# Optimization experiments

Measured on AMD Instinct MI355X. Metric: run time of the kernel, lower is better.

Reference implementation:

```python
import jax, jax.numpy as jnp
import numpy as np
import math

NUM_HEADS = 32
NUM_KV_HEADS = 8
HEAD_DIM = 128
HIDDEN = 4096
BATCH = 2
SEQ = 2048
MASK_MIN = -1e9


def _rope(x, cos, sin):
    # x: [B, S, H, D], cos/sin: [S, D/2]
    d2 = x.shape[-1] // 2
    x1, x2 = x[..., :d2], x[..., d2:]
    c = cos[None, :, None, :]
    s = sin[None, :, None, :]
    return jnp.concatenate([x1 * c - x2 * s, x2 * c + x1 * s], axis=-1)


def setup_inputs() -> dict:
    key = jax.random.key(0)
    k1, k2, k3 = jax.random.split(key, 3)
    hidden_states = jax.random.normal(k1, (BATCH, SEQ, HIDDEN), dtype=jnp.float32) * 0.02
    Wqkv = jax.random.normal(k2, (HIDDEN, (NUM_HEADS + 2 * NUM_KV_HEADS) * HEAD_DIM), dtype=jnp.float32) * (HIDDEN ** -0.5)
    Wo = jax.random.normal(k3, (NUM_HEADS * HEAD_DIM, HIDDEN), dtype=jnp.float32) * (HIDDEN ** -0.5)
    pos = np.arange(SEQ, dtype=np.float32)
    inv_freq = 1.0 / (10000.0 ** (np.arange(0, HEAD_DIM, 2, dtype=np.float32) / HEAD_DIM))
    freqs = np.outer(pos, inv_freq)  # [S, D/2]
    cos = jnp.asarray(np.cos(freqs), dtype=jnp.float32)
    sin = jnp.asarray(np.sin(freqs), dtype=jnp.float32)
    # causal additive mask [B, 1, S, S]
    causal = np.triu(np.full((SEQ, SEQ), MASK_MIN, dtype=np.float32), k=1)
    attention_mask = jnp.broadcast_to(jnp.asarray(causal)[None, None], (BATCH, 1, SEQ, SEQ))
    return {"hidden_states": hidden_states, "Wqkv": Wqkv, "Wo": Wo,
            "cos": cos, "sin": sin, "attention_mask": attention_mask}


def reference(hidden_states, Wqkv, Wo, cos, sin, attention_mask):
    B, S, H = hidden_states.shape
    n_rep = NUM_HEADS // NUM_KV_HEADS
    qkv = jnp.einsum('bsh,hd->bsd', hidden_states, Wqkv)
    q_end = NUM_HEADS * HEAD_DIM
    k_end = q_end + NUM_KV_HEADS * HEAD_DIM
    q = qkv[..., :q_end].reshape(B, S, NUM_HEADS, HEAD_DIM)
    k = qkv[..., q_end:k_end].reshape(B, S, NUM_KV_HEADS, HEAD_DIM)
    v = qkv[..., k_end:].reshape(B, S, NUM_KV_HEADS, HEAD_DIM)
    q = _rope(q, cos, sin)
    k = _rope(k, cos, sin)
    # repeat_kv: expand kv heads to query heads
    k = jnp.repeat(k, n_rep, axis=2)  # [B, S, NH, D]
    v = jnp.repeat(v, n_rep, axis=2)
    scores = jnp.einsum('bqhd,bkhd->bhqk', q, k) / math.sqrt(HEAD_DIM)
    scores = scores + attention_mask
    scores = jnp.maximum(scores, jnp.finfo(scores.dtype).min)
    probs = jax.nn.softmax(scores.astype(jnp.float32), axis=-1).astype(q.dtype)
    attn = jnp.einsum('bhqk,bkhd->bqhd', probs, v)  # [B, S, NH, D]
    attn = attn.reshape(B, S, NUM_HEADS * HEAD_DIM)
    return jnp.einsum('bsd,dh->bsh', attn, Wo)
```

## Files before the change

### kernel.cpp

```cpp
#include <hip/hip_runtime.h>

typedef unsigned short u16;
typedef __bf16 bf16x8 __attribute__((ext_vector_type(8)));
typedef float f32x4 __attribute__((ext_vector_type(4)));
typedef float f32x16 __attribute__((ext_vector_type(16)));
typedef u16 u16x4 __attribute__((ext_vector_type(4)));

#define SEQ 2048
#define NQKV 6144
#define HID 4096

__device__ inline u16 f2bf(float f) {
  union { float f; unsigned u; } x; x.f = f;
  unsigned r = x.u + 0x7fffu + ((x.u >> 16) & 1u);
  return (u16)(r >> 16);
}
__device__ inline float bf2f(u16 u) {
  union { unsigned u; float f; } x; x.u = ((unsigned)u) << 16;
  return x.f;
}
__device__ inline f32x4 mfma16(bf16x8 a, bf16x8 b, f32x4 c) {
  return __builtin_amdgcn_mfma_f32_16x16x32_bf16(a, b, c, 0, 0, 0);
}
__device__ inline f32x16 mfma32(bf16x8 a, bf16x8 b, f32x16 c) {
  return __builtin_amdgcn_mfma_f32_32x32x16_bf16(a, b, c, 0, 0, 0);
}
__device__ inline unsigned cvtpk(float lo, float hi) {
  unsigned r;
  asm("v_cvt_pk_bf16_f32 %0, %1, %2" : "=v"(r) : "v"(lo), "v"(hi));
  return r;
}
__device__ inline void gload16(const void* g, void* l) {
  __builtin_amdgcn_global_load_lds((const __attribute__((address_space(1))) void*)g,
                                   (__attribute__((address_space(3))) void*)l,
                                   16, 0, 0);
}


__global__ __launch_bounds__(256) void conv_kernel(const float* __restrict__ in,
                                                   u16* __restrict__ out) {
  int i = (blockIdx.x * 256 + threadIdx.x) * 4;
  int m = i >> 12, k = i & 4095;
  float4 v = *(const float4*)(in + i);
  u16x4 o;
  o[0] = f2bf(v.x); o[1] = f2bf(v.y); o[2] = f2bf(v.z); o[3] = f2bf(v.w);
  int p = m >> 8, r = m & 255;
  int t = k >> 5, kc = (k >> 3) & 3, e = k & 7;
  int slot = ((r >> 5) << 7) + (kc << 5) + (r & 31);
  *(u16x4*)(out + ((size_t)(p * 128 + t) * 1024 + slot) * 8 + e) = o;
}

__global__ __launch_bounds__(256) void transconv_qkv_kernel(const float* __restrict__ in,
                                                            u16* __restrict__ out) {
  __shared__ u16 tile[32][33];
  int c0 = blockIdx.x * 32, r0 = blockIdx.y * 32;
  int tx = threadIdx.x & 31, ty = threadIdx.x >> 5;
  for (int i = 0; i < 4; ++i)
    tile[ty + 8 * i][tx] = f2bf(in[(size_t)(r0 + ty + 8 * i) * NQKV + c0 + tx]);
  __syncthreads();
  int t = r0 >> 5;
  for (int i = 0; i < 4; ++i) {
    int n = c0 + ty + 8 * i;
    int p = n / 384, pc = n - p * 384;
    int kc = tx >> 3, e = tx & 7;
    int slot = ((pc >> 5) << 7) + (kc << 5) + (pc & 31);
    out[((size_t)(p * 128 + t) * 1536 + slot) * 8 + e] = tile[tx][ty + 8 * i];
  }
}

__global__ __launch_bounds__(256) void transconv_kernel(const float* __restrict__ in,
                                                        u16* __restrict__ out,
                                                        int R, int C) {
  __shared__ u16 tile[32][33];
  int c0 = blockIdx.x * 32, r0 = blockIdx.y * 32;
  int tx = threadIdx.x & 31, ty = threadIdx.x >> 5;
  for (int i = 0; i < 4; ++i)
    tile[ty + 8 * i][tx] = f2bf(in[(size_t)(r0 + ty + 8 * i) * C + c0 + tx]);
  __syncthreads();
  for (int i = 0; i < 4; ++i)
    out[(size_t)(c0 + ty + 8 * i) * R + r0 + tx] = tile[tx][ty + 8 * i];
}

__global__ __launch_bounds__(512, 2) void gemm32_kernel(const u16* __restrict__ At,
                                                        const u16* __restrict__ Btl,
                                                        u16* __restrict__ C,
                                                        int M, int N, int K, int nby) {
  __shared__ __align__(16) u16 As[3][256 * 32];
  __shared__ __align__(16) u16 Bs[3][384 * 32];
  int nwg = gridDim.x;
  int bid = blockIdx.x;
  int s = (bid & 7) * (nwg >> 3) + (bid >> 3);
  int by = s % nby, bx = s / nby;
  int row0 = by * 256, col0 = bx * 384;
  int tid = threadIdx.x, w = tid >> 6, l = tid & 63;
  int wm = w >> 2, wn = w & 3;
  int l31 = l & 31, lh = l >> 5;
  const u16* Ap = At + (size_t)by * 128 * 1024 * 8;
  const u16* Bp = Btl + (size_t)bx * 128 * 1536 * 8;
  int nkt = K >> 5;

  f32x16 acc[4][3] = {};

#define STA32(tt, bf)                                                         \
  { _Pragma("unroll")                                                         \
    for (int j = 0; j < 2; ++j) {                                             \
      int cid = j * 512 + tid;                                                \
      gload16(Ap + ((size_t)(tt) * 1024 + cid) * 8, &As[bf][cid * 8]);        \
    } }
#define STB32(tt, bf)                                                         \
  { _Pragma("unroll")                                                         \
    for (int j = 0; j < 3; ++j) {                                             \
      int cid = j * 512 + tid;                                                \
      gload16(Bp + ((size_t)(tt) * 1536 + cid) * 8, &Bs[bf][cid * 8]);        \
    } }
#define RA32(bf, im, ks, dst)                                                 \
  { int slot = ((wm * 4 + (im)) << 7) + (((ks) * 2 + lh) << 5) + l31;         \
    dst = *(const bf16x8*)&As[bf][slot * 8]; }
#define RB32(bf, in, ks, dst)                                                 \
  { int slot = ((wn * 3 + (in)) << 7) + (((ks) * 2 + lh) << 5) + l31;         \
    dst = *(const bf16x8*)&Bs[bf][slot * 8]; }

  STA32(0, 0); STB32(0, 0); STA32(1, 1); STB32(1, 1);
  asm volatile("s_waitcnt vmcnt(5)" ::: "memory");
  __builtin_amdgcn_s_barrier();

  int cur = 0;
  for (int t = 0; t < nkt; ++t) {
    int nb = cur + 2; if (nb >= 3) nb -= 3;
    bool pf = (t + 2 < nkt);
    bf16x8 a0, a1, a2, a3, b0, b1, b2;
    RA32(cur, 0, 0, a0); RA32(cur, 1, 0, a1); RA32(cur, 2, 0, a2); RA32(cur, 3, 0, a3);
    RB32(cur, 0, 0, b0); RB32(cur, 1, 0, b1); RB32(cur, 2, 0, b2);
    if (pf) STA32(t + 2, nb);
    __builtin_amdgcn_s_barrier();
    asm volatile("s_waitcnt lgkmcnt(0)" ::: "memory");
    __builtin_amdgcn_s_setprio(1);
    acc[0][0] = mfma32(a0, b0, acc[0][0]); acc[0][1] = mfma32(a0, b1, acc[0][1]);
    acc[0][2] = mfma32(a0, b2, acc[0][2]);
    acc[1][0] = mfma32(a1, b0, acc[1][0]); acc[1][1] = mfma32(a1, b1, acc[1][1]);
    acc[1][2] = mfma32(a1, b2, acc[1][2]);
    acc[2][0] = mfma32(a2, b0, acc[2][0]); acc[2][1] = mfma32(a2, b1, acc[2][1]);
    acc[2][2] = mfma32(a2, b2, acc[2][2]);
    acc[3][0] = mfma32(a3, b0, acc[3][0]); acc[3][1] = mfma32(a3, b1, acc[3][1]);
    acc[3][2] = mfma32(a3, b2, acc[3][2]);
    __builtin_amdgcn_s_setprio(0);
    __builtin_amdgcn_s_barrier();
    RA32(cur, 0, 1, a0); RA32(cur, 1, 1, a1); RA32(cur, 2, 1, a2); RA32(cur, 3, 1, a3);
    RB32(cur, 0, 1, b0); RB32(cur, 1, 1, b1); RB32(cur, 2, 1, b2);
    if (pf) STB32(t + 2, nb);
    __builtin_amdgcn_s_barrier();
    asm volatile("s_waitcnt lgkmcnt(0)" ::: "memory");
    __builtin_amdgcn_s_setprio(1);
    acc[0][0] = mfma32(a0, b0, acc[0][0]); acc[0][1] = mfma32(a0, b1, acc[0][1]);
    acc[0][2] = mfma32(a0, b2, acc[0][2]);
    acc[1][0] = mfma32(a1, b0, acc[1][0]); acc[1][1] = mfma32(a1, b1, acc[1][1]);
    acc[1][2] = mfma32(a1, b2, acc[1][2]);
    acc[2][0] = mfma32(a2, b0, acc[2][0]); acc[2][1] = mfma32(a2, b1, acc[2][1]);
    acc[2][2] = mfma32(a2, b2, acc[2][2]);
    acc[3][0] = mfma32(a3, b0, acc[3][0]); acc[3][1] = mfma32(a3, b1, acc[3][1]);
    acc[3][2] = mfma32(a3, b2, acc[3][2]);
    __builtin_amdgcn_s_setprio(0);
    if (pf)              { asm volatile("s_waitcnt vmcnt(5)" ::: "memory"); }
    else if (t + 1 < nkt){ asm volatile("s_waitcnt vmcnt(0)" ::: "memory"); }
    __builtin_amdgcn_s_barrier();
    cur = cur + 1 == 3 ? 0 : cur + 1;
  }
#undef STA32
#undef STB32
#undef RA32
#undef RB32

#pragma unroll
  for (int im = 0; im < 4; ++im)
#pragma unroll
    for (int in = 0; in < 3; ++in)
#pragma unroll
      for (int reg = 0; reg < 16; ++reg) {
        int row = row0 + wm * 128 + im * 32 + (reg & 3) + 8 * (reg >> 2) + 4 * lh;
        int col = col0 + wn * 96 + in * 32 + l31;
        C[(size_t)row * N + col] = f2bf(acc[im][in][reg]);
      }
}

__device__ inline void store_out(u16* p, float v) { *p = f2bf(v); }
__device__ inline void store_out(float* p, float v) { *p = v; }

template <typename OutT>
__global__ __launch_bounds__(512, 2) void gemm_kernel(const u16* __restrict__ A,
                                                      const u16* __restrict__ Bt,
                                                      OutT* __restrict__ C,
                                                      int M, int N, int K, int nby) {
  __shared__ __align__(16) u16 As[2][2][256 * 32];
  __shared__ __align__(16) u16 Bs[2][2][256 * 32];
  int nwg = gridDim.x;
  int bid = blockIdx.x;
  int s = (bid & 7) * (nwg >> 3) + (bid >> 3);
  int by = s % nby, bx = s / nby;
  int row0 = by * 256, col0 = bx * 256;
  int tid = threadIdx.x, w = tid >> 6, l = tid & 63;
  int wm = w >> 2, wn = w & 3;
  int lo = l & 15, hi = l >> 4;
  int sr = tid >> 2;
  int sc = tid & 3;
  int lc = sc ^ ((tid >> 3) & 3);
  const u16* Ab = A + (size_t)row0 * K;
  const u16* Bb = Bt + (size_t)col0 * K;
  int nkt = K >> 6;

  f32x4 acc[8][4] = {};

#define STA(tt, kh)                                                           \
  { _Pragma("unroll")                                                         \
    for (int j = 0; j < 2; ++j) {                                             \
      int row = j * 128 + sr;                                                 \
      gload16(Ab + (size_t)row * K + (tt) * 64 + (kh) * 32 + lc * 8,          \
              &As[(tt) & 1][kh][row * 32 + sc * 8]);                          \
    } }
#define STB(tt, kh)                                                           \
  { _Pragma("unroll")                                                         \
    for (int j = 0; j < 2; ++j) {                                             \
      int row = j * 128 + sr;                                                 \
      gload16(Bb + (size_t)row * K + (tt) * 64 + (kh) * 32 + lc * 8,          \
              &Bs[(tt) & 1][kh][row * 32 + sc * 8]);                          \
    } }
#define RA(cur, kh, fm, dst)                                                  \
  { int r = wm * 128 + (fm) * 16 + lo;                                        \
    dst = *(const bf16x8*)&As[cur][kh][r * 32 + ((hi ^ ((r >> 1) & 3)) * 8)]; }
#define RB(cur, kh, fn, dst)                                                  \
  { int r = wn * 64 + (fn) * 16 + lo;                                         \
    dst = *(const bf16x8*)&Bs[cur][kh][r * 32 + ((hi ^ ((r >> 1) & 3)) * 8)]; }

  STA(0, 0); STB(0, 0); STA(0, 1); STB(0, 1);
  asm volatile("s_waitcnt vmcnt(4)" ::: "memory");
  __builtin_amdgcn_s_barrier();

  bf16x8 af[4], bfr[4];
  for (int t = 0; t < nkt; ++t) {
    int cur = t & 1;
    bool pf = (t + 1 < nkt);
    RA(cur, 0, 0, af[0]); RA(cur, 0, 1, af[1]); RA(cur, 0, 2, af[2]); RA(cur, 0, 3, af[3]);
    RB(cur, 0, 0, bfr[0]); RB(cur, 0, 1, bfr[1]); RB(cur, 0, 2, bfr[2]); RB(cur, 0, 3, bfr[3]);
    if (pf) STA(t + 1, 0);
    __builtin_amdgcn_s_barrier();
    asm volatile("s_waitcnt lgkmcnt(0)" ::: "memory");
    __builtin_amdgcn_s_setprio(1);
#pragma unroll
    for (int fm = 0; fm < 4; ++fm)
#pragma unroll
      for (int fn = 0; fn < 4; ++fn)
        acc[fm][fn] = mfma16(af[fm], bfr[fn], acc[fm][fn]);
    __builtin_amdgcn_s_setprio(0);
    __builtin_amdgcn_s_barrier();
    RA(cur, 0, 4, af[0]); RA(cur, 0, 5, af[1]); RA(cur, 0, 6, af[2]); RA(cur, 0, 7, af[3]);
    if (pf) STB(t + 1, 0);
    __builtin_amdgcn_s_barrier();
    asm volatile("s_waitcnt lgkmcnt(0)" ::: "memory");
    __builtin_amdgcn_s_setprio(1);
#pragma unroll
    for (int fm = 0; fm < 4; ++fm)
#pragma unroll
      for (int fn = 0; fn < 4; ++fn)
        acc[4 + fm][fn] = mfma16(af[fm], bfr[fn], acc[4 + fm][fn]);
    __builtin_amdgcn_s_setprio(0);
    if (pf) { asm volatile("s_waitcnt vmcnt(4)" ::: "memory"); }
    else    { asm volatile("s_waitcnt vmcnt(0)" ::: "memory"); }
    __builtin_amdgcn_s_barrier();
    RA(cur, 1, 0, af[0]); RA(cur, 1, 1, af[1]); RA(cur, 1, 2, af[2]); RA(cur, 1, 3, af[3]);
    RB(cur, 1, 0, bfr[0]); RB(cur, 1, 1, bfr[1]); RB(cur, 1, 2, bfr[2]); RB(cur, 1, 3, bfr[3]);
    if (pf) STA(t + 1, 1);
    __builtin_amdgcn_s_barrier();
    asm volatile("s_waitcnt lgkmcnt(0)" ::: "memory");
    __builtin_amdgcn_s_setprio(1);
#pragma unroll
    for (int fm = 0; fm < 4; ++fm)
#pragma unroll
      for (int fn = 0; fn < 4; ++fn)
        acc[fm][fn] = mfma16(af[fm], bfr[fn], acc[fm][fn]);
    __builtin_amdgcn_s_setprio(0);
    __builtin_amdgcn_s_barrier();
    RA(cur, 1, 4, af[0]); RA(cur, 1, 5, af[1]); RA(cur, 1, 6, af[2]); RA(cur, 1, 7, af[3]);
    if (pf) STB(t + 1, 1);
    __builtin_amdgcn_s_barrier();
    asm volatile("s_waitcnt lgkmcnt(0)" ::: "memory");
    __builtin_amdgcn_s_setprio(1);
#pragma unroll
    for (int fm = 0; fm < 4; ++fm)
#pragma unroll
      for (int fn = 0; fn < 4; ++fn)
        acc[4 + fm][fn] = mfma16(af[fm], bfr[fn], acc[4 + fm][fn]);
    __builtin_amdgcn_s_setprio(0);
    if (pf) { asm volatile("s_waitcnt vmcnt(4)" ::: "memory"); }
    __builtin_amdgcn_s_barrier();
  }
#undef STA
#undef STB
#undef RA
#undef RB

  for (int fm = 0; fm < 8; ++fm)
    for (int fn = 0; fn < 4; ++fn)
      for (int rr = 0; rr < 4; ++rr) {
        int row = row0 + wm * 128 + fm * 16 + hi * 4 + rr;
        int col = col0 + wn * 64 + fn * 16 + lo;
        store_out(&C[(size_t)row * N + col], acc[fm][fn][rr]);
      }
}

__global__ __launch_bounds__(256) void rope_kernel(u16* __restrict__ qkv,
                                                   const float* __restrict__ cosb,
                                                   const float* __restrict__ sinb) {
  int idx = blockIdx.x * 256 + threadIdx.x;
  int d = idx & 63;
  int head = (idx >> 6) % 40;
  int m = idx / (64 * 40);
  int s = m & (SEQ - 1);
  int col = head < 32 ? head * 128 : 4096 + (head - 32) * 128;
  u16* p = qkv + (size_t)m * NQKV + col;
  float x1 = bf2f(p[d]), x2 = bf2f(p[d + 64]);
  float c = cosb[s * 64 + d], sn = sinb[s * 64 + d];
  p[d] = f2bf(x1 * c - x2 * sn);
  p[d + 64] = f2bf(x2 * c + x1 * sn);
}

__global__ __launch_bounds__(256) void vtrans_kernel(const u16* __restrict__ qkv,
                                                     u16* __restrict__ Vt) {
  __shared__ u16 tile[32][33];
  int bid = blockIdx.x;
  int dt = bid & 3;
  int st = (bid >> 2) & 63;
  int bk = bid >> 8;
  int b = bk >> 3, kvh = bk & 7;
  int tx = threadIdx.x & 31, ty = threadIdx.x >> 5;
  for (int i = 0; i < 4; ++i) {
    int s = st * 32 + ty + 8 * i;
    tile[ty + 8 * i][tx] = qkv[(size_t)(b * SEQ + s) * NQKV + 5120 + kvh * 128 + dt * 32 + tx];
  }
  __syncthreads();
  for (int i = 0; i < 4; ++i) {
    int d = dt * 32 + ty + 8 * i;
    Vt[((size_t)bk * 128 + d) * SEQ + st * 32 + tx] = tile[tx][ty + 8 * i];
  }
}

__global__ __launch_bounds__(256, 2) void flash_kernel(const u16* __restrict__ qkv,
                                                       const u16* __restrict__ Vt,
                                                       u16* __restrict__ attn) {
  const float C2 = 0.12751740f;
  int bid = blockIdx.x;
  int bh = bid & 63;
  int pr = bid >> 6;
  int h = bh & 31;
  int b = bh >> 5;
  int w = threadIdx.x >> 6, l = threadIdx.x & 63;
  int hv = l >> 5;
  int q32 = l & 31;
  int kvh = h >> 2;

  __shared__ __align__(16) u16 Ks[2][64 * 128];
  __shared__ __align__(16) u16 Vs[2][128 * 64];

  const u16* kb = qkv + (size_t)(b * SEQ) * NQKV + 4096 + kvh * 128;
  const u16* vtb = Vt + (size_t)(b * 8 + kvh) * 128 * SEQ;

#define STAGEKV(TT, BF)                                                       \
  { _Pragma("unroll")                                                         \
    for (int i = 0; i < 4; ++i) {                                             \
      int ck = w * 4 + i;                                                     \
      int rk = ck * 4 + (l >> 4);                                             \
      gload16(kb + (size_t)((TT) * 64 + rk) * NQKV + (((l & 15) ^ (rk & 7)) * 8), \
              &Ks[BF][ck * 512]);                                             \
      int rv = ck * 8 + (l >> 3);                                             \
      gload16(vtb + (size_t)rv * SEQ + (TT) * 64 + (((l & 7) ^ (rv & 7)) * 8), \
              &Vs[BF][ck * 512]);                                             \
    } }

  for (int pass = 0; pass < 2; ++pass) {
    int qc = pass ? 15 - pr : pr;
    int q0 = qc * 128 + w * 32;
    int qg = q0 + q32;
    __syncthreads();

    bf16x8 qf[8];
    {
      const u16* qr = qkv + (size_t)(b * SEQ + qg) * NQKV + h * 128 + hv * 8;
#pragma unroll
      for (int d0 = 0; d0 < 8; ++d0) qf[d0] = *(const bf16x8*)(qr + d0 * 16);
    }
    f32x16 o[4] = {};
    float mreg = -1e30f, lreg = 0.f;
    int ktend = 2 * qc + 1;
    int mykt = 2 * qc + (w >> 1);

    STAGEKV(0, 0);
    for (int kt = 0; kt <= ktend; ++kt) {
      int buf = kt & 1;
      if (kt < ktend) {
        STAGEKV(kt + 1, buf ^ 1);
        asm volatile("s_waitcnt vmcnt(8)" ::: "memory");
      } else {
        asm volatile("s_waitcnt vmcnt(0)" ::: "memory");
      }
      __builtin_amdgcn_s_barrier();

      if (kt <= mykt) {
        f32x16 s0 = {}, s1 = {};
        int swzk = q32 & 7;
#pragma unroll
        for (int d0 = 0; d0 < 8; ++d0) {
          int sl = (((d0 * 2 + hv) ^ swzk) * 8);
          bf16x8 k0 = *(const bf16x8*)&Ks[buf][q32 * 128 + sl];
          bf16x8 k1 = *(const bf16x8*)&Ks[buf][(32 + q32) * 128 + sl];
          s0 = mfma32(k0, qf[d0], s0);
          s1 = mfma32(k1, qf[d0], s1);
        }
        if (kt == mykt) {
#pragma unroll
          for (int r = 0; r < 16; ++r) {
            int kloc = (r & 3) + 8 * (r >> 2) + 4 * hv;
            if (kt * 64 + kloc > qg) s0[r] = -1e30f;
            if (kt * 64 + 32 + kloc > qg) s1[r] = -1e30f;
          }
        }
        float pm = -1e30f;
#pragma unroll
        for (int r = 0; r < 16; ++r) {
          pm = fmaxf(pm, s0[r]);
          pm = fmaxf(pm, s1[r]);
        }
        pm = fmaxf(pm, __shfl_xor(pm, 32));
        if (!__all(pm - mreg <= 62.746f)) {
          float mnew = fmaxf(mreg, pm);
          float al = exp2f((mreg - mnew) * C2);
          lreg *= al;
#pragma unroll
          for (int r = 0; r < 16; ++r) {
            o[0][r] *= al; o[1][r] *= al; o[2][r] *= al; o[3][r] *= al;
          }
          mreg = mnew;
        }
        float rs = 0.f;
#pragma unroll
        for (int r = 0; r < 16; ++r) {
          s0[r] = exp2f((s0[r] - mreg) * C2); rs += s0[r];
          s1[r] = exp2f((s1[r] - mreg) * C2); rs += s1[r];
        }
        rs += __shfl_xor(rs, 32);
        lreg += rs;
        bf16x8 pa[4];
#define MKPA(KSI, SP, RB)                                                     \
        { unsigned wA = cvtpk(SP[(RB) + 0], SP[(RB) + 1]);                    \
          unsigned wB = cvtpk(SP[(RB) + 2], SP[(RB) + 3]);                    \
          unsigned wC = cvtpk(SP[(RB) + 4], SP[(RB) + 5]);                    \
          unsigned wD = cvtpk(SP[(RB) + 6], SP[(RB) + 7]);                    \
          unsigned sA = __shfl_xor(wA, 32), sB = __shfl_xor(wB, 32);          \
          unsigned sC = __shfl_xor(wC, 32), sD = __shfl_xor(wD, 32);          \
          union { unsigned u[4]; bf16x8 v; } pk;                              \
          pk.u[0] = hv ? sC : wA; pk.u[1] = hv ? sD : wB;                     \
          pk.u[2] = hv ? wC : sA; pk.u[3] = hv ? wD : sB;                     \
          pa[KSI] = pk.v; }
        MKPA(0, s0, 0) MKPA(1, s0, 8) MKPA(2, s1, 0) MKPA(3, s1, 8)
#undef MKPA
#pragma unroll
        for (int db = 0; db < 4; ++db) {
          int rv = db * 32 + q32;
          int swz = rv & 7;
#pragma unroll
          for (int ks = 0; ks < 4; ++ks) {
            bf16x8 vf = *(const bf16x8*)&Vs[buf][rv * 64 + (((ks * 2 + hv) ^ swz) * 8)];
            o[db] = mfma32(vf, pa[ks], o[db]);
          }
        }
      }
    }
    float invl = 1.0f / lreg;
    u16* op = attn + (size_t)(b * SEQ + qg) * 4096 + h * 128 + hv * 4;
#pragma unroll
    for (int db = 0; db < 4; ++db)
#pragma unroll
      for (int g = 0; g < 4; ++g) {
        unsigned w0 = cvtpk(o[db][g * 4 + 0] * invl, o[db][g * 4 + 1] * invl);
        unsigned w1 = cvtpk(o[db][g * 4 + 2] * invl, o[db][g * 4 + 3] * invl);
        uint2 val; val.x = w0; val.y = w1;
        *(uint2*)(op + db * 32 + g * 8) = val;
      }
  }
#undef STAGEKV
}

extern "C" void kernel_launch(void* const* d_in, const int* in_sizes, int n_in,
                              void* d_out, int out_size, void* d_ws, size_t ws_size,
                              hipStream_t stream) {
  const float* hidden = (const float*)d_in[0];
  const float* Wqkv = (const float*)d_in[1];
  const float* Wo = (const float*)d_in[2];
  const float* cosb = (const float*)d_in[3];
  const float* sinb = (const float*)d_in[4];
  float* out = (float*)d_out;

  char* ws = (char*)d_ws;
  u16* R1 = (u16*)ws;
  u16* R2 = (u16*)(ws + 50331648);
  u16* R3 = (u16*)(ws + 100663296);

  conv_kernel<<<16384, 256, 0, stream>>>(hidden, R3);
  transconv_qkv_kernel<<<dim3(6144 / 32, 4096 / 32), 256, 0, stream>>>(Wqkv, R1);
  gemm32_kernel<<<256, 512, 0, stream>>>(R3, R1, R2, 4096, 6144, 4096, 16);
  rope_kernel<<<40960, 256, 0, stream>>>(R2, cosb, sinb);
  vtrans_kernel<<<4096, 256, 0, stream>>>(R2, R3);
  flash_kernel<<<512, 256, 0, stream>>>(R2, R3, R1);
  transconv_kernel<<<dim3(4096 / 32, 4096 / 32), 256, 0, stream>>>(Wo, R2, 4096, 4096);
  gemm_kernel<float><<<256, 512, 0, stream>>>(R1, R2, out, 4096, 4096, 4096, 16);
}
```

Before: 521.1 us.

## Use pre-tiled layout and 32x32 MFMA triple-buffered GEMM for output projection

The output projection now follows the same design as the QKV GEMM. The flash kernel writes attention output directly in a pre-tiled slot layout, and the Wo transpose-convert kernel emits the matching tiled layout. A new gemm32_o kernel then reads contiguous 16-byte chunks with 32x32x16 MFMAs and a 3-stage buffer ring, replacing the 16x16 double-buffered swizzled GEMM. The aim is to simplify LDS addressing, remove bank-conflict swizzles and deepen prefetch, at the cost of scattered stores in the flash epilogue.

```diff
diff --git a/kernel.cpp b/kernel.cpp
--- a/kernel.cpp
+++ b/kernel.cpp
@@ -18,9 +18,6 @@
 __device__ inline float bf2f(u16 u) {
   union { unsigned u; float f; } x; x.u = ((unsigned)u) << 16;
   return x.f;
-}
-__device__ inline f32x4 mfma16(bf16x8 a, bf16x8 b, f32x4 c) {
-  return __builtin_amdgcn_mfma_f32_16x16x32_bf16(a, b, c, 0, 0, 0);
 }
 __device__ inline f32x16 mfma32(bf16x8 a, bf16x8 b, f32x16 c) {
   return __builtin_amdgcn_mfma_f32_32x32x16_bf16(a, b, c, 0, 0, 0);
@@ -68,17 +65,22 @@
   }
 }
 
-__global__ __launch_bounds__(256) void transconv_kernel(const float* __restrict__ in,
-                                                        u16* __restrict__ out,
-                                                        int R, int C) {
+__global__ __launch_bounds__(256) void transconv_wo_kernel(const float* __restrict__ in,
+                                                           u16* __restrict__ out) {
   __shared__ u16 tile[32][33];
   int c0 = blockIdx.x * 32, r0 = blockIdx.y * 32;
   int tx = threadIdx.x & 31, ty = threadIdx.x >> 5;
   for (int i = 0; i < 4; ++i)
-    tile[ty + 8 * i][tx] = f2bf(in[(size_t)(r0 + ty + 8 * i) * C + c0 + tx]);
+    tile[ty + 8 * i][tx] = f2bf(in[(size_t)(r0 + ty + 8 * i) * HID + c0 + tx]);
   __syncthreads();
-  for (int i = 0; i < 4; ++i)
-    out[(size_t)(c0 + ty + 8 * i) * R + r0 + tx] = tile[tx][ty + 8 * i];
+  int t = r0 >> 5;
+  for (int i = 0; i < 4; ++i) {
+    int n = c0 + ty + 8 * i;
+    int p = n >> 8, pc = n & 255;
+    int kc = tx >> 3, e = tx & 7;
+    int slot = ((pc >> 5) << 7) + (kc << 5) + (pc & 31);
+    out[((size_t)(p * 128 + t) * 1024 + slot) * 8 + e] = tile[tx][ty + 8 * i];
+  }
 }
 
 __global__ __launch_bounds__(512, 2) void gemm32_kernel(const u16* __restrict__ At,
@@ -182,16 +184,12 @@
       }
 }
 
-__device__ inline void store_out(u16* p, float v) { *p = f2bf(v); }
-__device__ inline void store_out(float* p, float v) { *p = v; }
-
-template <typename OutT>
-__global__ __launch_bounds__(512, 2) void gemm_kernel(const u16* __restrict__ A,
-                                                      const u16* __restrict__ Bt,
-                                                      OutT* __restrict__ C,
-                                                      int M, int N, int K, int nby) {
-  __shared__ __align__(16) u16 As[2][2][256 * 32];
-  __shared__ __align__(16) u16 Bs[2][2][256 * 32];
+__global__ __launch_bounds__(512, 2) void gemm32_o_kernel(const u16* __restrict__ At,
+                                                          const u16* __restrict__ Btl,
+                                                          float* __restrict__ C,
+                                                          int M, int N, int K, int nby) {
+  __shared__ __align__(16) u16 As[3][256 * 32];
+  __shared__ __align__(16) u16 Bs[3][256 * 32];
   int nwg = gridDim.x;
   int bid = blockIdx.x;
   int s = (bid & 7) * (nwg >> 3) + (bid >> 3);
@@ -199,110 +197,83 @@
   int row0 = by * 256, col0 = bx * 256;
   int tid = threadIdx.x, w = tid >> 6, l = tid & 63;
   int wm = w >> 2, wn = w & 3;
-  int lo = l & 15, hi = l >> 4;
-  int sr = tid >> 2;
-  int sc = tid & 3;
-  int lc = sc ^ ((tid >> 3) & 3);
-  const u16* Ab = A + (size_t)row0 * K;
-  const u16* Bb = Bt + (size_t)col0 * K;
-  int nkt = K >> 6;
-
-  f32x4 acc[8][4] = {};
-
-#define STA(tt, kh)                                                           \
+  int l31 = l & 31, lh = l >> 5;
+  const u16* Ap = At + (size_t)by * 128 * 1024 * 8;
+  const u16* Bp = Btl + (size_t)bx * 128 * 1024 * 8;
+  int nkt = K >> 5;
+
+  f32x16 acc[4][2] = {};
+
+#define STAO(tt, bf)                                                          \
   { _Pragma("unroll")                                                         \
     for (int j = 0; j < 2; ++j) {                                             \
-      int row = j * 128 + sr;                                                 \
-      gload16(Ab + (size_t)row * K + (tt) * 64 + (kh) * 32 + lc * 8,          \
-              &As[(tt) & 1][kh][row * 32 + sc * 8]);                          \
+      int cid = j * 512 + tid;                                                \
+      gload16(Ap + ((size_t)(tt) * 1024 + cid) * 8, &As[bf][cid * 8]);        \
     } }
-#define STB(tt, kh)                                                           \
+#define STBO(tt, bf)                                                          \
   { _Pragma("unroll")                                                         \
     for (int j = 0; j < 2; ++j) {                                             \
-      int row = j * 128 + sr;                                                 \
-      gload16(Bb + (size_t)row * K + (tt) * 64 + (kh) * 32 + lc * 8,          \
-              &Bs[(tt) & 1][kh][row * 32 + sc * 8]);                          \
+      int cid = j * 512 + tid;                                                \
+      gload16(Bp + ((size_t)(tt) * 1024 + cid) * 8, &Bs[bf][cid * 8]);        \
     } }
-#define RA(cur, kh, fm, dst)                                                  \
-  { int r = wm * 128 + (fm) * 16 + lo;                                        \
-    dst = *(const bf16x8*)&As[cur][kh][r * 32 + ((hi ^ ((r >> 1) & 3)) * 8)]; }
-#define RB(cur, kh, fn, dst)                                                  \
-  { int r = wn * 64 + (fn) * 16 + lo;                                         \
-    dst = *(const bf16x8*)&Bs[cur][kh][r * 32 + ((hi ^ ((r >> 1) & 3)) * 8)]; }
-
-  STA(0, 0); STB(0, 0); STA(0, 1); STB(0, 1);
+#define RAO(bf, im, ks, dst)                                                  \
+  { int slot = ((wm * 4 + (im)) << 7) + (((ks) * 2 + lh) << 5) + l31;         \
+    dst = *(const bf16x8*)&As[bf][slot * 8]; }
+#define RBO(bf, in, ks, dst)                                                  \
+  { int slot = ((wn * 2 + (in)) << 7) + (((ks) * 2 + lh) << 5) + l31;         \
+    dst = *(const bf16x8*)&Bs[bf][slot * 8]; }
+
+  STAO(0, 0); STBO(0, 0); STAO(1, 1); STBO(1, 1);
   asm volatile("s_waitcnt vmcnt(4)" ::: "memory");
   __builtin_amdgcn_s_barrier();
 
-  bf16x8 af[4], bfr[4];
+  int cur = 0;
   for (int t = 0; t < nkt; ++t) {
-    int cur = t & 1;
-    bool pf = (t + 1 < nkt);
-    RA(cur, 0, 0, af[0]); RA(cur, 0, 1, af[1]); RA(cur, 0, 2, af[2]); RA(cur, 0, 3, af[3]);
-    RB(cur, 0, 0, bfr[0]); RB(cur, 0, 1, bfr[1]); RB(cur, 0, 2, bfr[2]); RB(cur, 0, 3, bfr[3]);
-    if (pf) STA(t + 1, 0);
+    int nb = cur + 2; if (nb >= 3) nb -= 3;
+    bool pf = (t + 2 < nkt);
+    bf16x8 a0, a1, a2, a3, b0, b1;
+    RAO(cur, 0, 0, a0); RAO(cur, 1, 0, a1); RAO(cur, 2, 0, a2); RAO(cur, 3, 0, a3);
+    RBO(cur, 0, 0, b0); RBO(cur, 1, 0, b1);
+    if (pf) STAO(t + 2, nb);
     __builtin_amdgcn_s_barrier();
     asm volatile("s_waitcnt lgkmcnt(0)" ::: "memory");
     __builtin_amdgcn_s_setprio(1);
-#pragma unroll
-    for (int fm = 0; fm < 4; ++fm)
-#pragma unroll
-      for (int fn = 0; fn < 4; ++fn)
-        acc[fm][fn] = mfma16(af[fm], bfr[fn], acc[fm][fn]);
+    acc[0][0] = mfma32(a0, b0, acc[0][0]); acc[0][1] = mfma32(a0, b1, acc[0][1]);
+    acc[1][0] = mfma32(a1, b0, acc[1][0]); acc[1][1] = mfma32(a1, b1, acc[1][1]);
+    acc[2][0] = mfma32(a2, b0, acc[2][0]); acc[2][1] = mfma32(a2, b1, acc[2][1]);
+    acc[3][0] = mfma32(a3, b0, acc[3][0]); acc[3][1] = mfma32(a3, b1, acc[3][1]);
     __builtin_amdgcn_s_setprio(0);
     __builtin_amdgcn_s_barrier();
-    RA(cur, 0, 4, af[0]); RA(cur, 0, 5, af[1]); RA(cur, 0, 6, af[2]); RA(cur, 0, 7, af[3]);
-    if (pf) STB(t + 1, 0);
+    RAO(cur, 0, 1, a0); RAO(cur, 1, 1, a1); RAO(cur, 2, 1, a2); RAO(cur, 3, 1, a3);
+    RBO(cur, 0, 1, b0); RBO(cur, 1, 1, b1);
+    if (pf) STBO(t + 2, nb);
     __builtin_amdgcn_s_barrier();
     asm volatile("s_waitcnt lgkmcnt(0)" ::: "memory");
     __builtin_amdgcn_s_setprio(1);
-#pragma unroll
-    for (int fm = 0; fm < 4; ++fm)
-#pragma unroll
-      for (int fn = 0; fn < 4; ++fn)
-        acc[4 + fm][fn] = mfma16(af[fm], bfr[fn], acc[4 + fm][fn]);
+    acc[0][0] = mfma32(a0, b0, acc[0][0]); acc[0][1] = mfma32(a0, b1, acc[0][1]);
+    acc[1][0] = mfma32(a1, b0, acc[1][0]); acc[1][1] = mfma32(a1, b1, acc[1][1]);
+    acc[2][0] = mfma32(a2, b0, acc[2][0]); acc[2][1] = mfma32(a2, b1, acc[2][1]);
+    acc[3][0] = mfma32(a3, b0, acc[3][0]); acc[3][1] = mfma32(a3, b1, acc[3][1]);
     __builtin_amdgcn_s_setprio(0);
-    if (pf) { asm volatile("s_waitcnt vmcnt(4)" ::: "memory"); }
-    else    { asm volatile("s_waitcnt vmcnt(0)" ::: "memory"); }
-    __builtin_amdgcn_s_barrier();
-    RA(cur, 1, 0, af[0]); RA(cur, 1, 1, af[1]); RA(cur, 1, 2, af[2]); RA(cur, 1, 3, af[3]);
-    RB(cur, 1, 0, bfr[0]); RB(cur, 1, 1, bfr[1]); RB(cur, 1, 2, bfr[2]); RB(cur, 1, 3, bfr[3]);
-    if (pf) STA(t + 1, 1);
-    __builtin_amdgcn_s_barrier();
-    asm volatile("s_waitcnt lgkmcnt(0)" ::: "memory");
-    __builtin_amdgcn_s_setprio(1);
-#pragma unroll
-    for (int fm = 0; fm < 4; ++fm)
-#pragma unroll
-      for (int fn = 0; fn < 4; ++fn)
-        acc[fm][fn] = mfma16(af[fm], bfr[fn], acc[fm][fn]);
-    __builtin_amdgcn_s_setprio(0);
-    __builtin_amdgcn_s_barrier();
-    RA(cur, 1, 4, af[0]); RA(cur, 1, 5, af[1]); RA(cur, 1, 6, af[2]); RA(cur, 1, 7, af[3]);
-    if (pf) STB(t + 1, 1);
-    __builtin_amdgcn_s_barrier();
-    asm volatile("s_waitcnt lgkmcnt(0)" ::: "memory");
-    __builtin_amdgcn_s_setprio(1);
-#pragma unroll
-    for (int fm = 0; fm < 4; ++fm)
-#pragma unroll
-      for (int fn = 0; fn < 4; ++fn)
-        acc[4 + fm][fn] = mfma16(af[fm], bfr[fn], acc[4 + fm][fn]);
-    __builtin_amdgcn_s_setprio(0);
-    if (pf) { asm volatile("s_waitcnt vmcnt(4)" ::: "memory"); }
-    __builtin_amdgcn_s_barrier();
-  }
-#undef STA
-#undef STB
-#undef RA
-#undef RB
-
-  for (int fm = 0; fm < 8; ++fm)
-    for (int fn = 0; fn < 4; ++fn)
-      for (int rr = 0; rr < 4; ++rr) {
-        int row = row0 + wm * 128 + fm * 16 + hi * 4 + rr;
-        int col = col0 + wn * 64 + fn * 16 + lo;
-        store_out(&C[(size_t)row * N + col], acc[fm][fn][rr]);
+    if (pf)              { asm volatile("s_waitcnt vmcnt(4)" ::: "memory"); }
+    else if (t + 1 < nkt){ asm volatile("s_waitcnt vmcnt(0)" ::: "memory"); }
+    __builtin_amdgcn_s_barrier();
+    cur = cur + 1 == 3 ? 0 : cur + 1;
+  }
+#undef STAO
+#undef STBO
+#undef RAO
+#undef RBO
+
+#pragma unroll
+  for (int im = 0; im < 4; ++im)
+#pragma unroll
+    for (int in = 0; in < 2; ++in)
+#pragma unroll
+      for (int reg = 0; reg < 16; ++reg) {
+        int row = row0 + wm * 128 + im * 32 + (reg & 3) + 8 * (reg >> 2) + 4 * lh;
+        int col = col0 + wn * 64 + in * 32 + l31;
+        C[(size_t)row * N + col] = acc[im][in][reg];
       }
 }
 
@@ -344,7 +315,7 @@
 
 __global__ __launch_bounds__(256, 2) void flash_kernel(const u16* __restrict__ qkv,
                                                        const u16* __restrict__ Vt,
-                                                       u16* __restrict__ attn) {
+                                                       u16* __restrict__ attnT) {
   const float C2 = 0.12751740f;
   int bid = blockIdx.x;
   int bh = bid & 63;
@@ -473,16 +444,21 @@
       }
     }
     float invl = 1.0f / lreg;
-    u16* op = attn + (size_t)(b * SEQ + qg) * 4096 + h * 128 + hv * 4;
-#pragma unroll
-    for (int db = 0; db < 4; ++db)
-#pragma unroll
-      for (int g = 0; g < 4; ++g) {
-        unsigned w0 = cvtpk(o[db][g * 4 + 0] * invl, o[db][g * 4 + 1] * invl);
-        unsigned w1 = cvtpk(o[db][g * 4 + 2] * invl, o[db][g * 4 + 3] * invl);
-        uint2 val; val.x = w0; val.y = w1;
-        *(uint2*)(op + db * 32 + g * 8) = val;
-      }
+    {
+      int m = b * SEQ + qg;
+      int p = m >> 8, r = m & 255;
+      u16* op = attnT + ((size_t)(p * 128 + h * 4) * 1024 +
+                         ((r >> 5) << 7) + (r & 31)) * 8 + 4 * hv;
+#pragma unroll
+      for (int db = 0; db < 4; ++db)
+#pragma unroll
+        for (int g = 0; g < 4; ++g) {
+          unsigned w0 = cvtpk(o[db][g * 4 + 0] * invl, o[db][g * 4 + 1] * invl);
+          unsigned w1 = cvtpk(o[db][g * 4 + 2] * invl, o[db][g * 4 + 3] * invl);
+          uint2 val; val.x = w0; val.y = w1;
+          *(uint2*)(op + db * 8192 + g * 256) = val;
+        }
+    }
   }
 #undef STAGEKV
 }
@@ -508,6 +484,6 @@
   rope_kernel<<<40960, 256, 0, stream>>>(R2, cosb, sinb);
   vtrans_kernel<<<4096, 256, 0, stream>>>(R2, R3);
   flash_kernel<<<512, 256, 0, stream>>>(R2, R3, R1);
-  transconv_kernel<<<dim3(4096 / 32, 4096 / 32), 256, 0, stream>>>(Wo, R2, 4096, 4096);
-  gemm_kernel<float><<<256, 512, 0, stream>>>(R1, R2, out, 4096, 4096, 4096, 16);
-}
+  transconv_wo_kernel<<<dim3(4096 / 32, 4096 / 32), 256, 0, stream>>>(Wo, R2);
+  gemm32_o_kernel<<<256, 512, 0, stream>>>(R1, R2, out, 4096, 4096, 4096, 16);
+}
```

Result: no change. 522.7 us (+0.3%).
